# Kernel optimization log

Hardware: AMD Instinct MI355X
Metric: run time of the kernel (lower is better)

Reference implementation:

```python
import jax, jax.numpy as jnp
import numpy as np


def setup_inputs() -> dict:
    key = jax.random.key(0)
    k1, k2 = jax.random.split(key)
    B, T, D = 8, 2048, 2048
    layer_in = jax.random.normal(k1, (B, T, D), dtype=jnp.float32)
    # nn.Linear(2D, 2D): weight [out=2D, in=2D], bias [2D]
    W_gate = jax.random.normal(k2, (2 * D, 2 * D), dtype=jnp.float32) * 0.02
    b_gate = jnp.zeros((2 * D,), dtype=jnp.float32)
    return {"layer_in": layer_in, "W_gate": W_gate, "b_gate": b_gate}


def reference(layer_in, W_gate, b_gate):
    # Cumulative average: tril(ones)/row_index @ x  ==  cumsum(x)/[1..t]
    t = layer_in.shape[1]
    denom = jnp.arange(1, t + 1, dtype=layer_in.dtype)[:, None]  # (t, 1)
    average_out = jnp.cumsum(layer_in, axis=1) / denom  # (B, t, D)
    # Gating: Linear(2D -> 2D) on concat(x, avg), then chunk into two gates
    gating_in = jnp.concatenate([layer_in, average_out], axis=-1)  # (B, t, 2D)
    gates = jnp.einsum('btk,ok->bto', gating_in, W_gate) + b_gate  # (B, t, 2D)
    input_gate, forget_gate = jnp.split(gates, 2, axis=2)
    gating_out = (jax.nn.sigmoid(input_gate) * layer_in
                  + jax.nn.sigmoid(forget_gate) * average_out)
    return gating_out, average_out
```

## Files before the change

kernel.cpp:

```cpp
#include <hip/hip_runtime.h>
#include <hip/hip_bf16.h>


#define Bb 8
#define Tt 2048
#define Dd 2048
#define Mm (Bb * Tt)
#define Kk 4096
#define NC 32
#define CT 64

typedef __bf16 bf16x8 __attribute__((ext_vector_type(8)));
typedef float f32x4 __attribute__((ext_vector_type(4)));

__device__ __forceinline__ void gload16(const void* g, void* l) {
    __builtin_amdgcn_global_load_lds(
        (const __attribute__((address_space(1))) unsigned int*)g,
        (__attribute__((address_space(3))) unsigned int*)l, 16, 0, 0);
}

__global__ void wconv_kernel(const float* __restrict__ W,
                             unsigned short* __restrict__ Wb, long n) {
    long i = ((long)blockIdx.x * blockDim.x + threadIdx.x) * 4;
    long stride = (long)gridDim.x * blockDim.x * 4;
    for (; i < n; i += stride) {
        float4 v = *(const float4*)(W + i);
        __hip_bfloat16 a = __float2bfloat16(v.x);
        __hip_bfloat16 b = __float2bfloat16(v.y);
        __hip_bfloat16 c = __float2bfloat16(v.z);
        __hip_bfloat16 d = __float2bfloat16(v.w);
        ushort4 u;
        u.x = *(unsigned short*)&a; u.y = *(unsigned short*)&b;
        u.z = *(unsigned short*)&c; u.w = *(unsigned short*)&d;
        *(ushort4*)(Wb + i) = u;
    }
}

__global__ void ksum_kernel(const float* __restrict__ X, float* __restrict__ S) {
    int d = blockIdx.y * 256 + threadIdx.x;
    int bc = blockIdx.x;
    int b = bc >> 5, c = bc & 31;
    const float* p = X + ((long)(b * Tt + c * CT)) * Dd + d;
    float s = 0.f;
#pragma unroll 8
    for (int t = 0; t < CT; ++t) s += p[(long)t * Dd];
    S[(long)bc * Dd + d] = s;
}

__global__ void kscan_kernel(const float* __restrict__ X, const float* __restrict__ S,
                             float* __restrict__ AVG, unsigned short* __restrict__ Gin) {
    int d = blockIdx.y * 256 + threadIdx.x;
    int bc = blockIdx.x;
    int b = bc >> 5, c = bc & 31;
    const float* Sp = S + (long)(b * NC) * Dd + d;
    float run = 0.f;
    for (int cc = 0; cc < c; ++cc) run += Sp[(long)cc * Dd];
    const float* p = X + ((long)(b * Tt + c * CT)) * Dd + d;
    long row = (long)b * Tt + c * CT;
    for (int tt = 0; tt < CT; ++tt) {
        float x = p[(long)tt * Dd];
        run += x;
        float av = run / (float)(c * CT + tt + 1);
        long r = row + tt;
        AVG[r * Dd + d] = av;
        __hip_bfloat16 xb = __float2bfloat16(x);
        __hip_bfloat16 ab = __float2bfloat16(av);
        Gin[r * 4096 + d] = *(unsigned short*)&xb;
        Gin[r * 4096 + 2048 + d] = *(unsigned short*)&ab;
    }
}

#define MFMA(va, vb, c_) c_ = __builtin_amdgcn_mfma_f32_16x16x32_bf16(va, vb, c_, 0, 0, 0)
#define RD(p_, i_) (*(const bf16x8*)((p_) + (i_) * 1024))
#define SBAR __builtin_amdgcn_s_barrier()
#define SCHB __builtin_amdgcn_sched_barrier(0)
#define LGKM0 asm volatile("s_waitcnt lgkmcnt(0)" ::: "memory")

#define CL_LO(A0_, A1_, A2_, A3_, B0_, B1_, B2_, B3_)                           \
    __builtin_amdgcn_s_setprio(1);                                              \
    MFMA(A0_,B0_,acc[0][0]); MFMA(A0_,B1_,acc[0][1]); MFMA(A0_,B2_,acc[0][2]); MFMA(A0_,B3_,acc[0][3]); \
    MFMA(A1_,B0_,acc[1][0]); MFMA(A1_,B1_,acc[1][1]); MFMA(A1_,B2_,acc[1][2]); MFMA(A1_,B3_,acc[1][3]); \
    MFMA(A2_,B0_,acc[2][0]); MFMA(A2_,B1_,acc[2][1]); MFMA(A2_,B2_,acc[2][2]); MFMA(A2_,B3_,acc[2][3]); \
    MFMA(A3_,B0_,acc[3][0]); MFMA(A3_,B1_,acc[3][1]); MFMA(A3_,B2_,acc[3][2]); MFMA(A3_,B3_,acc[3][3]); \
    __builtin_amdgcn_s_setprio(0);
#define CL_HI(A4_, A5_, A6_, A7_, B0_, B1_, B2_, B3_)                           \
    __builtin_amdgcn_s_setprio(1);                                              \
    MFMA(A4_,B0_,acc[4][0]); MFMA(A4_,B1_,acc[4][1]); MFMA(A4_,B2_,acc[4][2]); MFMA(A4_,B3_,acc[4][3]); \
    MFMA(A5_,B0_,acc[5][0]); MFMA(A5_,B1_,acc[5][1]); MFMA(A5_,B2_,acc[5][2]); MFMA(A5_,B3_,acc[5][3]); \
    MFMA(A6_,B0_,acc[6][0]); MFMA(A6_,B1_,acc[6][1]); MFMA(A6_,B2_,acc[6][2]); MFMA(A6_,B3_,acc[6][3]); \
    MFMA(A7_,B0_,acc[7][0]); MFMA(A7_,B1_,acc[7][1]); MFMA(A7_,B2_,acc[7][2]); MFMA(A7_,B3_,acc[7][3]); \
    __builtin_amdgcn_s_setprio(0);

#define TILE64(t_, bb_, STG_, V1_, V3_)                                         \
  {                                                                             \
    const char* pa_ = rA0 + (bb_);                                              \
    const char* pb_ = rB0 + (bb_);                                              \
    char* nb_ = ldsb + ((bb_) ^ 65536) + woff;                                  \
    const long ko_ = ((long)(t_) + 1) * 128;                                    \
          \
    bf16x8 a0 = RD(pa_,0), a1 = RD(pa_,1), a2 = RD(pa_,2), a3 = RD(pa_,3);      \
    bf16x8 b0 = RD(pb_,0), b1 = RD(pb_,1), b2 = RD(pb_,2), b3 = RD(pb_,3);      \
    if (STG_) { gload16(gA0 + ko_, nb_); gload16(gA1 + ko_, nb_ + 8192); }      \
    SCHB; SBAR; LGKM0; SCHB;                                                    \
    CL_LO(a0, a1, a2, a3, b0, b1, b2, b3)                                       \
    SCHB; SBAR;                                                                 \
       \
    bf16x8 a4 = RD(pa_,4), a5 = RD(pa_,5), a6 = RD(pa_,6), a7 = RD(pa_,7);      \
    if (STG_) { gload16(gB0 + ko_, nb_ + 16384); gload16(gB1 + ko_, nb_ + 24576); } \
    SCHB; SBAR; LGKM0; SCHB;                                                    \
    CL_HI(a4, a5, a6, a7, b0, b1, b2, b3)                                       \
    SCHB;                                                                       \
    asm volatile("s_waitcnt vmcnt(" #V1_ ")" ::: "memory");                     \
    SBAR;                                                                       \
          \
    bf16x8 c0 = RD(pa_+32768,0), c1 = RD(pa_+32768,1), c2 = RD(pa_+32768,2), c3 = RD(pa_+32768,3); \
    bf16x8 d0 = RD(pb_+32768,0), d1 = RD(pb_+32768,1), d2 = RD(pb_+32768,2), d3 = RD(pb_+32768,3); \
    if (STG_) { gload16(gA0 + ko_ + 64, nb_ + 32768); gload16(gA1 + ko_ + 64, nb_ + 40960); } \
    SCHB; SBAR; LGKM0; SCHB;                                                    \
    CL_LO(c0, c1, c2, c3, d0, d1, d2, d3)                                       \
    SCHB; SBAR;                                                                 \
       \
    bf16x8 c4 = RD(pa_+32768,4), c5 = RD(pa_+32768,5), c6 = RD(pa_+32768,6), c7 = RD(pa_+32768,7); \
    if (STG_) { gload16(gB0 + ko_ + 64, nb_ + 49152); gload16(gB1 + ko_ + 64, nb_ + 57344); } \
    SCHB; SBAR; LGKM0; SCHB;                                                    \
    CL_HI(c4, c5, c6, c7, d0, d1, d2, d3)                                       \
    SCHB;                                                                       \
    asm volatile("s_waitcnt vmcnt(" #V3_ ")" ::: "memory");                     \
    SBAR;                                                                       \
  }

__global__ __launch_bounds__(512, 1) void gemm64_kernel(
    const unsigned short* __restrict__ Gin,
    const unsigned short* __restrict__ Wb,
    const float* __restrict__ bias,
    float* __restrict__ OUT)
{
    __shared__ __attribute__((aligned(128))) char lds[131072];
    char* ldsb = (char*)lds;

    const int tid = threadIdx.x;
    const int w = tid >> 6, l = tid & 63;
    const int wm = w >> 2, wn = w & 3;
    const int lm = l & 15;
    const int woff = w * 1024;

    const int bid = blockIdx.x;
    const int batch = bid >> 8;
    const int rr = bid & 255;
    const int xcd = rr & 7;
    const int j = rr >> 3;
    const int nt = xcd * 2 + (j >> 4);
    const int mt = batch * 16 + (j & 15);
    const long m0 = (long)mt * 256;
    const int n0 = nt * 128;

    const int srow = tid >> 2;
    const int schunk = (tid & 3) ^ ((tid >> 3) & 3);
    const char* gA0 = (const char*)Gin + (m0 + srow) * 8192 + schunk * 16;
    const char* gA1 = gA0 + 128 * 8192;
    const long jr0 = n0 + ((srow >> 6) << 5) + (srow & 31) + (((srow >> 5) & 1) << 11);
    const int j1 = 128 + srow;
    const long jr1 = n0 + ((j1 >> 6) << 5) + (j1 & 31) + (((j1 >> 5) & 1) << 11);
    const char* gB0 = (const char*)Wb + jr0 * 8192 + schunk * 16;
    const char* gB1 = (const char*)Wb + jr1 * 8192 + schunk * 16;

    const int cbyte = (((l >> 4) ^ ((lm >> 1) & 3))) * 16;
    const char* rA0 = ldsb + (wm * 128 + lm) * 64 + cbyte;
    const char* rB0 = ldsb + 16384 + (wn * 64 + lm) * 64 + cbyte;

    f32x4 acc[8][4] = {};

    gload16(gA0,      ldsb + woff);
    gload16(gA1,      ldsb + 8192 + woff);
    gload16(gB0,      ldsb + 16384 + woff);
    gload16(gB1,      ldsb + 24576 + woff);
    gload16(gA0 + 64, ldsb + 32768 + woff);
    gload16(gA1 + 64, ldsb + 40960 + woff);
    gload16(gB0 + 64, ldsb + 49152 + woff);
    gload16(gB1 + 64, ldsb + 57344 + woff);
    asm volatile("s_waitcnt vmcnt(4)" ::: "memory");
    SBAR; SCHB;

#pragma unroll 1
    for (int t = 0; t < 62; t += 2) {
        TILE64(t,     0,     1, 4, 4)
        TILE64(t + 1, 65536, 1, 4, 4)
    }
    TILE64(62, 0,     1, 4, 4)
    TILE64(63, 65536, 0, 0, 0)

#pragma unroll
    for (int mi = 0; mi < 8; ++mi) {
        long rbase = m0 + wm * 128 + mi * 16 + (l >> 4) * 4;
#pragma unroll
        for (int nj = 0; nj < 2; ++nj) {
            int d = n0 + wn * 32 + nj * 16 + lm;
            float bi_ = bias[d];
            float bf_ = bias[d + 2048];
#pragma unroll
            for (int r = 0; r < 4; ++r) {
                long row = rbase + r;
                unsigned int ux = Gin[row * 4096 + d];
                unsigned int ua = Gin[row * 4096 + 2048 + d];
                union { unsigned int u; float f; } cx, ca;
                cx.u = ux << 16; ca.u = ua << 16;
                float gi = acc[mi][nj][r] + bi_;
                float gf = acc[mi][nj + 2][r] + bf_;
                float si = 1.f / (1.f + __expf(-gi));
                float sf = 1.f / (1.f + __expf(-gf));
                OUT[row * 2048 + d] = si * cx.f + sf * ca.f;
            }
        }
    }
}

extern "C" void kernel_launch(void* const* d_in, const int* in_sizes, int n_in,
                              void* d_out, int out_size, void* d_ws, size_t ws_size,
                              hipStream_t stream) {
    const float* X = (const float*)d_in[0];
    const float* W = (const float*)d_in[1];
    const float* bias = (const float*)d_in[2];

    float* OUT = (float*)d_out;
    float* AVG = OUT + (long)Mm * Dd;

    char* ws = (char*)d_ws;
    unsigned short* Wb  = (unsigned short*)ws;
    unsigned short* Gin = (unsigned short*)(ws + 33554432);
    float* S = (float*)(ws + 33554432 + 134217728);

    wconv_kernel<<<2048, 256, 0, stream>>>(W, Wb, (long)Kk * Kk);
    ksum_kernel<<<dim3(Bb * NC, Dd / 256), 256, 0, stream>>>(X, S);
    kscan_kernel<<<dim3(Bb * NC, Dd / 256), 256, 0, stream>>>(X, S, AVG, Gin);
    gemm64_kernel<<<1024, 512, 0, stream>>>(Gin, Wb, bias, OUT);
}
```

Baseline: 615.6 us.

## Software-pipeline LDS fragment loads under MFMA clusters and remove extra barriers

Restructures the GEMM main loop so the next A-fragment LDS reads are issued before the current MFMA cluster runs, using persistent register fragments instead of per-cluster locals. Most workgroup barriers are removed, leaving one per 32-wide K half, and the vmcnt waits are retuned. The aim is to hide LDS latency behind matrix-core work and cut barrier stalls. It holds more live fragment registers and depends on the looser synchronisation still ordering LDS buffer reuse correctly.

```diff
diff --git a/kernel.cpp b/kernel.cpp
--- a/kernel.cpp
+++ b/kernel.cpp
@@ -74,62 +74,67 @@
 #define RD(p_, i_) (*(const bf16x8*)((p_) + (i_) * 1024))
 #define SBAR __builtin_amdgcn_s_barrier()
 #define SCHB __builtin_amdgcn_sched_barrier(0)
-#define LGKM0 asm volatile("s_waitcnt lgkmcnt(0)" ::: "memory")
-
-#define CL_LO(A0_, A1_, A2_, A3_, B0_, B1_, B2_, B3_)                           \
+#define LGKM0 do { asm volatile("s_waitcnt lgkmcnt(0)" ::: "memory"); SCHB; } while (0)
+
+#define CL_LO(B0_, B1_, B2_, B3_)                                               \
     __builtin_amdgcn_s_setprio(1);                                              \
-    MFMA(A0_,B0_,acc[0][0]); MFMA(A0_,B1_,acc[0][1]); MFMA(A0_,B2_,acc[0][2]); MFMA(A0_,B3_,acc[0][3]); \
-    MFMA(A1_,B0_,acc[1][0]); MFMA(A1_,B1_,acc[1][1]); MFMA(A1_,B2_,acc[1][2]); MFMA(A1_,B3_,acc[1][3]); \
-    MFMA(A2_,B0_,acc[2][0]); MFMA(A2_,B1_,acc[2][1]); MFMA(A2_,B2_,acc[2][2]); MFMA(A2_,B3_,acc[2][3]); \
-    MFMA(A3_,B0_,acc[3][0]); MFMA(A3_,B1_,acc[3][1]); MFMA(A3_,B2_,acc[3][2]); MFMA(A3_,B3_,acc[3][3]); \
+    MFMA(aL0,B0_,acc[0][0]); MFMA(aL0,B1_,acc[0][1]); MFMA(aL0,B2_,acc[0][2]); MFMA(aL0,B3_,acc[0][3]); \
+    MFMA(aL1,B0_,acc[1][0]); MFMA(aL1,B1_,acc[1][1]); MFMA(aL1,B2_,acc[1][2]); MFMA(aL1,B3_,acc[1][3]); \
+    MFMA(aL2,B0_,acc[2][0]); MFMA(aL2,B1_,acc[2][1]); MFMA(aL2,B2_,acc[2][2]); MFMA(aL2,B3_,acc[2][3]); \
+    MFMA(aL3,B0_,acc[3][0]); MFMA(aL3,B1_,acc[3][1]); MFMA(aL3,B2_,acc[3][2]); MFMA(aL3,B3_,acc[3][3]); \
     __builtin_amdgcn_s_setprio(0);
-#define CL_HI(A4_, A5_, A6_, A7_, B0_, B1_, B2_, B3_)                           \
+#define CL_HI(B0_, B1_, B2_, B3_)                                               \
     __builtin_amdgcn_s_setprio(1);                                              \
-    MFMA(A4_,B0_,acc[4][0]); MFMA(A4_,B1_,acc[4][1]); MFMA(A4_,B2_,acc[4][2]); MFMA(A4_,B3_,acc[4][3]); \
-    MFMA(A5_,B0_,acc[5][0]); MFMA(A5_,B1_,acc[5][1]); MFMA(A5_,B2_,acc[5][2]); MFMA(A5_,B3_,acc[5][3]); \
-    MFMA(A6_,B0_,acc[6][0]); MFMA(A6_,B1_,acc[6][1]); MFMA(A6_,B2_,acc[6][2]); MFMA(A6_,B3_,acc[6][3]); \
-    MFMA(A7_,B0_,acc[7][0]); MFMA(A7_,B1_,acc[7][1]); MFMA(A7_,B2_,acc[7][2]); MFMA(A7_,B3_,acc[7][3]); \
+    MFMA(aH0,B0_,acc[4][0]); MFMA(aH0,B1_,acc[4][1]); MFMA(aH0,B2_,acc[4][2]); MFMA(aH0,B3_,acc[4][3]); \
+    MFMA(aH1,B0_,acc[5][0]); MFMA(aH1,B1_,acc[5][1]); MFMA(aH1,B2_,acc[5][2]); MFMA(aH1,B3_,acc[5][3]); \
+    MFMA(aH2,B0_,acc[6][0]); MFMA(aH2,B1_,acc[6][1]); MFMA(aH2,B2_,acc[6][2]); MFMA(aH2,B3_,acc[6][3]); \
+    MFMA(aH3,B0_,acc[7][0]); MFMA(aH3,B1_,acc[7][1]); MFMA(aH3,B2_,acc[7][2]); MFMA(aH3,B3_,acc[7][3]); \
     __builtin_amdgcn_s_setprio(0);
 
-#define TILE64(t_, bb_, STG_, V1_, V3_)                                         \
+#define TILE64(t_, bb_, STG_, VM_, VB_)                                         \
   {                                                                             \
     const char* pa_ = rA0 + (bb_);                                              \
     const char* pb_ = rB0 + (bb_);                                              \
     char* nb_ = ldsb + ((bb_) ^ 65536) + woff;                                  \
     const long ko_ = ((long)(t_) + 1) * 128;                                    \
-          \
-    bf16x8 a0 = RD(pa_,0), a1 = RD(pa_,1), a2 = RD(pa_,2), a3 = RD(pa_,3);      \
-    bf16x8 b0 = RD(pb_,0), b1 = RD(pb_,1), b2 = RD(pb_,2), b3 = RD(pb_,3);      \
+                         \
+    aL0 = RD(pa_,0); aL1 = RD(pa_,1); aL2 = RD(pa_,2); aL3 = RD(pa_,3);         \
+    bb0 = RD(pb_,0); bb1 = RD(pb_,1); bb2 = RD(pb_,2); bb3 = RD(pb_,3);         \
     if (STG_) { gload16(gA0 + ko_, nb_); gload16(gA1 + ko_, nb_ + 8192); }      \
-    SCHB; SBAR; LGKM0; SCHB;                                                    \
-    CL_LO(a0, a1, a2, a3, b0, b1, b2, b3)                                       \
-    SCHB; SBAR;                                                                 \
-       \
-    bf16x8 a4 = RD(pa_,4), a5 = RD(pa_,5), a6 = RD(pa_,6), a7 = RD(pa_,7);      \
+    LGKM0;                                                         \
+                                      \
+    aH0 = RD(pa_,4); aH1 = RD(pa_,5); aH2 = RD(pa_,6); aH3 = RD(pa_,7);         \
+    SCHB;                                                                       \
+    CL_LO(bb0, bb1, bb2, bb3)                                                   \
+    SCHB;                                                                       \
+    asm volatile("s_waitcnt vmcnt(" #VM_ ")" ::: "memory");                     \
+    SBAR; SCHB;                                             \
+    LGKM0;                                                         \
+             \
+    aL0 = RD(pa_+32768,0); aL1 = RD(pa_+32768,1); aL2 = RD(pa_+32768,2); aL3 = RD(pa_+32768,3); \
+    bd0 = RD(pb_+32768,0); bd1 = RD(pb_+32768,1); bd2 = RD(pb_+32768,2); bd3 = RD(pb_+32768,3); \
     if (STG_) { gload16(gB0 + ko_, nb_ + 16384); gload16(gB1 + ko_, nb_ + 24576); } \
-    SCHB; SBAR; LGKM0; SCHB;                                                    \
-    CL_HI(a4, a5, a6, a7, b0, b1, b2, b3)                                       \
-    SCHB;                                                                       \
-    asm volatile("s_waitcnt vmcnt(" #V1_ ")" ::: "memory");                     \
-    SBAR;                                                                       \
-          \
-    bf16x8 c0 = RD(pa_+32768,0), c1 = RD(pa_+32768,1), c2 = RD(pa_+32768,2), c3 = RD(pa_+32768,3); \
-    bf16x8 d0 = RD(pb_+32768,0), d1 = RD(pb_+32768,1), d2 = RD(pb_+32768,2), d3 = RD(pb_+32768,3); \
+    SCHB;                                                                       \
+    CL_HI(bb0, bb1, bb2, bb3)                                                   \
+    SCHB;                                                                       \
+    LGKM0;                                                         \
+                     \
+    aH0 = RD(pa_+32768,4); aH1 = RD(pa_+32768,5); aH2 = RD(pa_+32768,6); aH3 = RD(pa_+32768,7); \
     if (STG_) { gload16(gA0 + ko_ + 64, nb_ + 32768); gload16(gA1 + ko_ + 64, nb_ + 40960); } \
-    SCHB; SBAR; LGKM0; SCHB;                                                    \
-    CL_LO(c0, c1, c2, c3, d0, d1, d2, d3)                                       \
-    SCHB; SBAR;                                                                 \
-       \
-    bf16x8 c4 = RD(pa_+32768,4), c5 = RD(pa_+32768,5), c6 = RD(pa_+32768,6), c7 = RD(pa_+32768,7); \
+    SCHB;                                                                       \
+    CL_LO(bd0, bd1, bd2, bd3)                                                   \
+    SCHB;                                                                       \
+    LGKM0;                                                         \
+                                         \
     if (STG_) { gload16(gB0 + ko_ + 64, nb_ + 49152); gload16(gB1 + ko_ + 64, nb_ + 57344); } \
-    SCHB; SBAR; LGKM0; SCHB;                                                    \
-    CL_HI(c4, c5, c6, c7, d0, d1, d2, d3)                                       \
-    SCHB;                                                                       \
-    asm volatile("s_waitcnt vmcnt(" #V3_ ")" ::: "memory");                     \
-    SBAR;                                                                       \
+    SCHB;                                                                       \
+    CL_HI(bd0, bd1, bd2, bd3)                                                   \
+    SCHB;                                                                       \
+    asm volatile("s_waitcnt vmcnt(" #VB_ ")" ::: "memory");                     \
+    SBAR; SCHB;                                           \
   }
 
-__global__ __launch_bounds__(512, 1) void gemm64_kernel(
+__global__ __launch_bounds__(512, 1) void gemmsp_kernel(
     const unsigned short* __restrict__ Gin,
     const unsigned short* __restrict__ Wb,
     const float* __restrict__ bias,
@@ -169,6 +174,9 @@
     const char* rB0 = ldsb + 16384 + (wn * 64 + lm) * 64 + cbyte;
 
     f32x4 acc[8][4] = {};
+
+    bf16x8 aL0, aL1, aL2, aL3, aH0, aH1, aH2, aH3;
+    bf16x8 bb0, bb1, bb2, bb3, bd0, bd1, bd2, bd3;
 
     gload16(gA0,      ldsb + woff);
     gload16(gA1,      ldsb + 8192 + woff);
@@ -183,10 +191,10 @@
 
 #pragma unroll 1
     for (int t = 0; t < 62; t += 2) {
-        TILE64(t,     0,     1, 4, 4)
-        TILE64(t + 1, 65536, 1, 4, 4)
-    }
-    TILE64(62, 0,     1, 4, 4)
+        TILE64(t,     0,     1, 2, 4)
+        TILE64(t + 1, 65536, 1, 2, 4)
+    }
+    TILE64(62, 0,     1, 2, 4)
     TILE64(63, 65536, 0, 0, 0)
 
 #pragma unroll
@@ -232,5 +240,5 @@
     wconv_kernel<<<2048, 256, 0, stream>>>(W, Wb, (long)Kk * Kk);
     ksum_kernel<<<dim3(Bb * NC, Dd / 256), 256, 0, stream>>>(X, S);
     kscan_kernel<<<dim3(Bb * NC, Dd / 256), 256, 0, stream>>>(X, S, AVG, Gin);
-    gemm64_kernel<<<1024, 512, 0, stream>>>(Gin, Wb, bias, OUT);
-}
+    gemmsp_kernel<<<1024, 512, 0, stream>>>(Gin, Wb, bias, OUT);
+}
```

Measured after the change: 609.7 us. Within noise of the previous version (-1.0%).
